# Kernel optimization log

Measured on AMD Instinct MI355X. Metric: run time of the kernel, lower is better.

Reference implementation:

```python
import jax, jax.numpy as jnp
import numpy as np

EPS = 1e-5


def setup_inputs() -> dict:
    key = jax.random.key(0)
    ks = jax.random.split(key, 7)
    N, M, D, H, DM = 8192, 128, 64, 8, 1024  # tokens, num_memories, d_memory, heads, d_model
    return {
        "query": jax.random.normal(ks[0], (N, DM), dtype=jnp.float32),
        "addresses": jax.random.normal(ks[1], (M, D), dtype=jnp.float32),
        "memories": jax.random.normal(ks[2], (N, M, D), dtype=jnp.float32),
        "Wq": jax.random.normal(ks[3], (DM, H * D), dtype=jnp.float32) / np.sqrt(DM),
        "bq": jax.random.normal(ks[4], (H * D,), dtype=jnp.float32) * 0.01,
        "Wo": jax.random.normal(ks[5], (H * D, DM), dtype=jnp.float32) / np.sqrt(H * D),
        "bo": jax.random.normal(ks[6], (DM,), dtype=jnp.float32) * 0.01,
    }


def reference(query, addresses, memories, Wq, bq, Wo, bo):
    N = query.shape[0]
    M, D = addresses.shape
    # Query projection -> heads: (N, H, D)
    q = (query @ Wq + bq).reshape(N, -1, D)
    q = jax.nn.relu(q)  # kernel feature map on query
    # Keys: memory content + learned addresses, kernel feature map
    k = jax.nn.relu(memories + addresses)  # (N, M, D)
    # make_kernel: contract over the num_memories dim
    matrix = jnp.einsum("nmd,nme->nde", k, memories)  # (N, D, D)
    normalizer = jnp.sum(k, axis=-2)  # (N, D)
    # read_from_kernel
    numerator = jnp.einsum("nhd,nde->nhe", q, matrix)  # (N, H, D)
    denominator = jnp.einsum("nhd,nd->nh", q, normalizer)[..., None] + EPS
    attn = numerator / denominator  # (N, H, D)
    # merge heads back to d_model
    return attn.reshape(N, -1) @ Wo + bo
```

## Files before the change

### kernel.cpp

```cpp
#include <hip/hip_runtime.h>

typedef __bf16 bf16x8 __attribute__((ext_vector_type(8)));
typedef __bf16 bf16x4 __attribute__((ext_vector_type(4)));
typedef __bf16 bf16x2 __attribute__((ext_vector_type(2)));
typedef float  f32x4  __attribute__((ext_vector_type(4)));

__device__ __forceinline__ void gload_lds16(const void* g, void* l) {
    auto gp = reinterpret_cast<const __attribute__((address_space(1))) unsigned int*>(
        reinterpret_cast<uintptr_t>(g));
    auto lp = reinterpret_cast<__attribute__((address_space(3))) unsigned int*>(
        reinterpret_cast<uintptr_t>(l));
    __builtin_amdgcn_global_load_lds(gp, lp, 16, 0, 0);
}

__device__ __forceinline__ void xcd_remap(int lin, int& bx, int& by) {
    const int wgid = (lin & 7) * 64 + (lin >> 3);
    bx = wgid & 7;
    by = wgid >> 3;
}

__global__ __launch_bounds__(256) void prep_all(
    const float* __restrict__ Wq, const float* __restrict__ Wo,
    const float* __restrict__ adr,
    __bf16* __restrict__ WqT, __bf16* __restrict__ WoT,
    __bf16* __restrict__ adrb)
{
    __shared__ float tile[32][33];
    const int bid = blockIdx.x, tid = threadIdx.x;

    if (bid < 1024) {
        const float* src; __bf16* dst; int R, C, r0, c0;
        if (bid < 512) {
            src = Wq; dst = WqT; R = 1024; C = 512;
            c0 = (bid & 15) * 32; r0 = (bid >> 4) * 32;
        } else {
            const int b = bid - 512;
            src = Wo; dst = WoT; R = 512; C = 1024;
            c0 = (b & 31) * 32; r0 = (b >> 5) * 32;
        }
        const int tx = tid & 31, ty = tid >> 5;
        #pragma unroll
        for (int i = ty; i < 32; i += 8)
            tile[i][tx] = src[(size_t)(r0 + i) * C + c0 + tx];
        __syncthreads();
        #pragma unroll
        for (int i = ty; i < 32; i += 8)
            dst[(size_t)(c0 + i) * R + r0 + tx] = (__bf16)tile[tx][i];
    } else {
        const int i = (bid - 1024) * 256 + tid;
        f32x4 a = ((const f32x4*)adr)[2 * i];
        f32x4 b = ((const f32x4*)adr)[2 * i + 1];
        bf16x8 o;
        #pragma unroll
        for (int j = 0; j < 4; ++j) { o[j] = (__bf16)a[j]; o[4 + j] = (__bf16)b[j]; }
        ((bf16x8*)adrb)[i] = o;
    }
}

__global__ __launch_bounds__(512) void gemm_qproj(
    const float* __restrict__ A, const __bf16* __restrict__ BT,
    const float* __restrict__ bias, __bf16* __restrict__ Out,
    int M, int N, int K)
{
    __shared__ __bf16 As[2][128][40];
    __shared__ __bf16 Bs[2][64][32];

    const int tid = threadIdx.x, lane = tid & 63, w = tid >> 6;
    const int wm = w >> 1, wn = w & 1;
    int bx, by;
    xcd_remap(blockIdx.x + 8 * blockIdx.y, bx, by);
    const int m0 = by * 128, n0 = bx * 64;
    const int r = lane & 15, g = lane >> 4;

    const int arow = tid >> 2, ac8 = (tid & 3) * 8;
    const float*  gA = A + (size_t)(m0 + arow) * K + ac8;
    const __bf16* gB = BT + (size_t)(n0 + 16 * w + (lane >> 2)) * K + (lane & 3) * 8;

    f32x4 acc[2][2];
    const f32x4 zero = {0.f, 0.f, 0.f, 0.f};
    #pragma unroll
    for (int mi = 0; mi < 2; ++mi)
        #pragma unroll
        for (int ni = 0; ni < 2; ++ni) acc[mi][ni] = zero;

    const int NT = K / 32;

    if (w < 4) gload_lds16(gB, &Bs[0][16 * w][0]);
    {
        const f32x4 la0 = *(const f32x4*)(gA);
        const f32x4 la1 = *(const f32x4*)(gA + 4);
        bf16x8 bl;
        #pragma unroll
        for (int j = 0; j < 4; ++j) { bl[j] = (__bf16)la0[j]; bl[4 + j] = (__bf16)la1[j]; }
        *(bf16x8*)&As[0][arow][ac8] = bl;
    }
    __syncthreads();

    int cur = 0;
    for (int t = 0; t < NT; ++t) {
        const int k0 = t * 32;
        f32x4 ln0, ln1;
        if (t + 1 < NT) {
            if (w < 4) gload_lds16(gB + k0 + 32, &Bs[cur ^ 1][16 * w][0]);
            ln0 = *(const f32x4*)(gA + k0 + 32);
            ln1 = *(const f32x4*)(gA + k0 + 36);
        }
        bf16x8 af[2], bfr[2];
        #pragma unroll
        for (int mi = 0; mi < 2; ++mi)
            af[mi] = *(const bf16x8*)&As[cur][wm * 32 + mi * 16 + r][g * 8];
        #pragma unroll
        for (int ni = 0; ni < 2; ++ni)
            bfr[ni] = *(const bf16x8*)&Bs[cur][wn * 32 + ni * 16 + r][g * 8];
        #pragma unroll
        for (int mi = 0; mi < 2; ++mi)
            #pragma unroll
            for (int ni = 0; ni < 2; ++ni)
                acc[mi][ni] = __builtin_amdgcn_mfma_f32_16x16x32_bf16(
                    af[mi], bfr[ni], acc[mi][ni], 0, 0, 0);
        if (t + 1 < NT) {
            bf16x8 bl;
            #pragma unroll
            for (int j = 0; j < 4; ++j) { bl[j] = (__bf16)ln0[j]; bl[4 + j] = (__bf16)ln1[j]; }
            *(bf16x8*)&As[cur ^ 1][arow][ac8] = bl;
        }
        __syncthreads();
        cur ^= 1;
    }

    const int orow = m0 + wm * 32 + g * 4;
    const int ocol = n0 + wn * 32 + r;
    #pragma unroll
    for (int ni = 0; ni < 2; ++ni) {
        const float bb = bias[ocol + ni * 16];
        #pragma unroll
        for (int mi = 0; mi < 2; ++mi) {
            #pragma unroll
            for (int q = 0; q < 4; ++q) {
                float v = fmaxf(acc[mi][ni][q] + bb, 0.f);
                Out[(size_t)(orow + mi * 16 + q) * N + ocol + ni * 16] = (__bf16)v;
            }
        }
    }
}

__global__ __launch_bounds__(512) void gemm_oproj(
    const __bf16* __restrict__ A, const __bf16* __restrict__ BT,
    const float* __restrict__ bias, float* __restrict__ Out,
    int M, int N, int K)
{
    __shared__ __bf16 As[2][128][32];
    __shared__ __bf16 Bs[2][128][32];

    const int tid = threadIdx.x, lane = tid & 63, w = tid >> 6;
    const int wm = w >> 1, wn = w & 1;
    int bx, by;
    xcd_remap(blockIdx.x + 8 * blockIdx.y, bx, by);
    const int m0 = by * 128, n0 = bx * 128;
    const int r = lane & 15, g = lane >> 4;

    const int srow = lane >> 2;
    const int scol = (lane & 3) * 8;
    const __bf16* gA = A  + (size_t)(m0 + 16 * w + srow) * K + scol;
    const __bf16* gB = BT + (size_t)(n0 + 16 * w + srow) * K + scol;

    f32x4 acc[2][4];
    const f32x4 zero = {0.f, 0.f, 0.f, 0.f};
    #pragma unroll
    for (int mi = 0; mi < 2; ++mi)
        #pragma unroll
        for (int ni = 0; ni < 4; ++ni) acc[mi][ni] = zero;

    const int NT = K / 32;

    gload_lds16(gA, &As[0][16 * w][0]);
    gload_lds16(gB, &Bs[0][16 * w][0]);
    __syncthreads();

    int cur = 0;
    for (int t = 0; t < NT; ++t) {
        const int k0 = t * 32;
        if (t + 1 < NT) {
            gload_lds16(gA + k0 + 32, &As[cur ^ 1][16 * w][0]);
            gload_lds16(gB + k0 + 32, &Bs[cur ^ 1][16 * w][0]);
        }
        bf16x8 af[2], bfr[4];
        #pragma unroll
        for (int mi = 0; mi < 2; ++mi)
            af[mi] = *(const bf16x8*)&As[cur][wm * 32 + mi * 16 + r][g * 8];
        #pragma unroll
        for (int ni = 0; ni < 4; ++ni)
            bfr[ni] = *(const bf16x8*)&Bs[cur][wn * 64 + ni * 16 + r][g * 8];
        #pragma unroll
        for (int mi = 0; mi < 2; ++mi)
            #pragma unroll
            for (int ni = 0; ni < 4; ++ni)
                acc[mi][ni] = __builtin_amdgcn_mfma_f32_16x16x32_bf16(
                    af[mi], bfr[ni], acc[mi][ni], 0, 0, 0);
        __syncthreads();
        cur ^= 1;
    }

    const int orow = m0 + wm * 32 + g * 4;
    const int ocol = n0 + wn * 64 + r;
    #pragma unroll
    for (int ni = 0; ni < 4; ++ni) {
        const float bb = bias[ocol + ni * 16];
        #pragma unroll
        for (int mi = 0; mi < 2; ++mi) {
            #pragma unroll
            for (int q = 0; q < 4; ++q) {
                Out[(size_t)(orow + mi * 16 + q) * N + ocol + ni * 16]
                    = acc[mi][ni][q] + bb;
            }
        }
    }
}

__device__ __forceinline__ int kbyte(int m, int e) {
    return m * 128 + ((((e >> 3) ^ (m & 7))) << 4) + (e & 7) * 2;
}

__global__ void memory_attn_mfma(
    const __bf16* __restrict__ Q,
    const float*  __restrict__ mem,
    const __bf16* __restrict__ adrb,
    __bf16* __restrict__ attn)
{
    __shared__ __align__(16) unsigned char kbuf[4][4096];
    __shared__ __align__(16) unsigned char tbuf[4][5120];
    __shared__ float denl[4][8];

    const int tid = threadIdx.x, lane = tid & 63, w = tid >> 6;
    const int n = blockIdx.x * 4 + w;
    const int v = lane & 15, g = lane >> 4;

    unsigned char* kb = kbuf[w];
    unsigned char* tb = tbuf[w];

    const __bf16* qp = Q + (size_t)n * 512 + v * 64 + 8 * g;
    const bf16x8 qf0 = *(const bf16x8*)(qp);
    const bf16x8 qf1 = *(const bf16x8*)(qp + 32);

    f32x4 acc[4];
    const f32x4 zero = {0.f, 0.f, 0.f, 0.f};
    #pragma unroll
    for (int nb = 0; nb < 4; ++nb) acc[nb] = zero;
    float psum = 0.f;

    for (int c = 0; c < 4; ++c) {
        const int mb = c * 32;
        #pragma unroll
        for (int i = 0; i < 4; ++i) {
            const int mo = 8 * i + 2 * g;
            const int e  = 4 * v;
            const float* pm = mem + (((size_t)n * 128 + mb + mo) * 64 + e);
            const f32x4 m0 = *(const f32x4*)pm;
            const f32x4 m1 = *(const f32x4*)(pm + 64);
            const bf16x4 a0 = *(const bf16x4*)(adrb + (size_t)(mb + mo) * 64 + e);
            const bf16x4 a1 = *(const bf16x4*)(adrb + (size_t)(mb + mo + 1) * 64 + e);
            bf16x4 k0, k1;
            #pragma unroll
            for (int j = 0; j < 4; ++j) {
                k0[j] = (__bf16)fmaxf(m0[j] + (float)a0[j], 0.f);
                k1[j] = (__bf16)fmaxf(m1[j] + (float)a1[j], 0.f);
            }
            *(bf16x4*)(kb + kbyte(mo,     e)) = k0;
            *(bf16x4*)(kb + kbyte(mo + 1, e)) = k1;
            const int kap = 8 * ((mo >> 2) & 3) + 4 * (mo >> 4) + (mo & 3);
            #pragma unroll
            for (int j2 = 0; j2 < 4; ++j2) {
                bf16x2 p = { (__bf16)m0[j2], (__bf16)m1[j2] };
                *(bf16x2*)(tb + (size_t)(e + j2) * 80 + kap * 2) = p;
            }
        }

        f32x4 sA0 = zero, sA1 = zero;
        {
            const bf16x8 a00 = *(const bf16x8*)(kb + kbyte(v,      8 * g));
            const bf16x8 a01 = *(const bf16x8*)(kb + kbyte(v,      32 + 8 * g));
            const bf16x8 a10 = *(const bf16x8*)(kb + kbyte(v + 16, 8 * g));
            const bf16x8 a11 = *(const bf16x8*)(kb + kbyte(v + 16, 32 + 8 * g));
            sA0 = __builtin_amdgcn_mfma_f32_16x16x32_bf16(a00, qf0, sA0, 0, 0, 0);
            sA0 = __builtin_amdgcn_mfma_f32_16x16x32_bf16(a01, qf1, sA0, 0, 0, 0);
            sA1 = __builtin_amdgcn_mfma_f32_16x16x32_bf16(a10, qf0, sA1, 0, 0, 0);
            sA1 = __builtin_amdgcn_mfma_f32_16x16x32_bf16(a11, qf1, sA1, 0, 0, 0);
        }
        psum += sA0[0] + sA0[1] + sA0[2] + sA0[3]
              + sA1[0] + sA1[1] + sA1[2] + sA1[3];

        bf16x8 pa;
        #pragma unroll
        for (int q = 0; q < 4; ++q) {
            pa[q]     = (__bf16)sA0[q];
            pa[4 + q] = (__bf16)sA1[q];
        }

        #pragma unroll
        for (int nb = 0; nb < 4; ++nb) {
            const bf16x8 bf = *(const bf16x8*)(tb + (size_t)(16 * nb + v) * 80 + 16 * g);
            acc[nb] = __builtin_amdgcn_mfma_f32_16x16x32_bf16(pa, bf, acc[nb], 0, 0, 0);
        }
    }

    psum += __shfl_xor(psum, 16);
    psum += __shfl_xor(psum, 32);
    if (lane < 8) denl[w][lane] = psum;

    if (g < 2) {
        const f32x4 d4 = *(const f32x4*)&denl[w][4 * g];
        float inv[4];
        #pragma unroll
        for (int q = 0; q < 4; ++q) inv[q] = 1.f / (d4[q] + 1e-5f);
        #pragma unroll
        for (int nb = 0; nb < 4; ++nb) {
            #pragma unroll
            for (int q = 0; q < 4; ++q) {
                attn[(size_t)n * 512 + (4 * g + q) * 64 + 16 * nb + v] =
                    (__bf16)(acc[nb][q] * inv[q]);
            }
        }
    }
}

extern "C" void kernel_launch(void* const* d_in, const int* in_sizes, int n_in,
                              void* d_out, int out_size, void* d_ws, size_t ws_size,
                              hipStream_t stream)
{
    const float* query     = (const float*)d_in[0];
    const float* addresses = (const float*)d_in[1];
    const float* memories  = (const float*)d_in[2];
    const float* Wq        = (const float*)d_in[3];
    const float* bq        = (const float*)d_in[4];
    const float* Wo        = (const float*)d_in[5];
    const float* bo        = (const float*)d_in[6];
    float* out = (float*)d_out;

    char* ws = (char*)d_ws;
    __bf16* WqT  = (__bf16*)(ws);
    __bf16* WoT  = (__bf16*)(ws + (1 << 20));
    __bf16* Qb   = (__bf16*)(ws + (2 << 20));
    __bf16* Ab   = (__bf16*)(ws + (10 << 20));
    __bf16* Adrb = (__bf16*)(ws + (18 << 20));

    prep_all<<<1028, 256, 0, stream>>>(Wq, Wo, addresses, WqT, WoT, Adrb);

    gemm_qproj<<<dim3(512 / 64, 8192 / 128), 512, 0, stream>>>(
        query, WqT, bq, Qb, 8192, 512, 1024);

    memory_attn_mfma<<<dim3(8192 / 4), 256, 0, stream>>>(Qb, memories, Adrb, Ab);

    gemm_oproj<<<dim3(1024 / 128, 8192 / 128), 512, 0, stream>>>(
        Ab, WoT, bo, out, 8192, 1024, 512);
}
```

Before: 113.8 us.

## Deepen prefetch pipelines in projection GEMMs with fine-grained waitcnt barriers

```diff
diff --git a/kernel.cpp b/kernel.cpp
--- a/kernel.cpp
+++ b/kernel.cpp
@@ -11,6 +11,25 @@
     auto lp = reinterpret_cast<__attribute__((address_space(3))) unsigned int*>(
         reinterpret_cast<uintptr_t>(l));
     __builtin_amdgcn_global_load_lds(gp, lp, 16, 0, 0);
+}
+
+__device__ __forceinline__ void barrier_lgkm() {
+    __builtin_amdgcn_sched_barrier(0);
+    asm volatile("s_waitcnt lgkmcnt(0)" ::: "memory");
+    __builtin_amdgcn_s_barrier();
+    __builtin_amdgcn_sched_barrier(0);
+}
+__device__ __forceinline__ void barrier_vm2_lgkm() {
+    __builtin_amdgcn_sched_barrier(0);
+    asm volatile("s_waitcnt vmcnt(2) lgkmcnt(0)" ::: "memory");
+    __builtin_amdgcn_s_barrier();
+    __builtin_amdgcn_sched_barrier(0);
+}
+__device__ __forceinline__ void barrier_vm0_lgkm() {
+    __builtin_amdgcn_sched_barrier(0);
+    asm volatile("s_waitcnt vmcnt(0) lgkmcnt(0)" ::: "memory");
+    __builtin_amdgcn_s_barrier();
+    __builtin_amdgcn_sched_barrier(0);
 }
 
 __device__ __forceinline__ void xcd_remap(int lin, int& bx, int& by) {
@@ -73,8 +92,10 @@
     const int r = lane & 15, g = lane >> 4;
 
     const int arow = tid >> 2, ac8 = (tid & 3) * 8;
-    const float*  gA = A + (size_t)(m0 + arow) * K + ac8;
-    const __bf16* gB = BT + (size_t)(n0 + 16 * w + (lane >> 2)) * K + (lane & 3) * 8;
+    const float* gA = A + (size_t)(m0 + arow) * K + ac8;
+    const bool bstage = (w < 4);
+    const int brow = 16 * (w & 3) + (lane >> 2), bc8 = (lane & 3) * 8;
+    const __bf16* gB = BT + (size_t)(n0 + brow) * K + bc8;
 
     f32x4 acc[2][2];
     const f32x4 zero = {0.f, 0.f, 0.f, 0.f};
@@ -85,33 +106,36 @@
 
     const int NT = K / 32;
 
-    if (w < 4) gload_lds16(gB, &Bs[0][16 * w][0]);
+    f32x4 pa0[2], pa1[2];
+    bf16x8 pb[2];
+
+    pa0[0] = *(const f32x4*)(gA);      pa1[0] = *(const f32x4*)(gA + 4);
+    pa0[1] = *(const f32x4*)(gA + 32); pa1[1] = *(const f32x4*)(gA + 36);
+    if (bstage) { pb[0] = *(const bf16x8*)(gB); pb[1] = *(const bf16x8*)(gB + 32); }
     {
-        const f32x4 la0 = *(const f32x4*)(gA);
-        const f32x4 la1 = *(const f32x4*)(gA + 4);
         bf16x8 bl;
         #pragma unroll
-        for (int j = 0; j < 4; ++j) { bl[j] = (__bf16)la0[j]; bl[4 + j] = (__bf16)la1[j]; }
+        for (int j = 0; j < 4; ++j) { bl[j] = (__bf16)pa0[0][j]; bl[4 + j] = (__bf16)pa1[0][j]; }
         *(bf16x8*)&As[0][arow][ac8] = bl;
-    }
-    __syncthreads();
-
-    int cur = 0;
+        if (bstage) *(bf16x8*)&Bs[0][brow][bc8] = pb[0];
+    }
+    barrier_lgkm();
+
+    #pragma unroll 2
     for (int t = 0; t < NT; ++t) {
-        const int k0 = t * 32;
-        f32x4 ln0, ln1;
-        if (t + 1 < NT) {
-            if (w < 4) gload_lds16(gB + k0 + 32, &Bs[cur ^ 1][16 * w][0]);
-            ln0 = *(const f32x4*)(gA + k0 + 32);
-            ln1 = *(const f32x4*)(gA + k0 + 36);
+        const int ph = t & 1;
+        if (t + 2 < NT) {
+            pa0[ph] = *(const f32x4*)(gA + (t + 2) * 32);
+            pa1[ph] = *(const f32x4*)(gA + (t + 2) * 32 + 4);
+            if (bstage) pb[ph] = *(const bf16x8*)(gB + (t + 2) * 32);
         }
         bf16x8 af[2], bfr[2];
         #pragma unroll
         for (int mi = 0; mi < 2; ++mi)
-            af[mi] = *(const bf16x8*)&As[cur][wm * 32 + mi * 16 + r][g * 8];
+            af[mi] = *(const bf16x8*)&As[ph][wm * 32 + mi * 16 + r][g * 8];
         #pragma unroll
         for (int ni = 0; ni < 2; ++ni)
-            bfr[ni] = *(const bf16x8*)&Bs[cur][wn * 32 + ni * 16 + r][g * 8];
+            bfr[ni] = *(const bf16x8*)&Bs[ph][wn * 32 + ni * 16 + r][g * 8];
         #pragma unroll
         for (int mi = 0; mi < 2; ++mi)
             #pragma unroll
@@ -121,11 +145,14 @@
         if (t + 1 < NT) {
             bf16x8 bl;
             #pragma unroll
-            for (int j = 0; j < 4; ++j) { bl[j] = (__bf16)ln0[j]; bl[4 + j] = (__bf16)ln1[j]; }
-            *(bf16x8*)&As[cur ^ 1][arow][ac8] = bl;
-        }
-        __syncthreads();
-        cur ^= 1;
+            for (int j = 0; j < 4; ++j) {
+                bl[j]     = (__bf16)pa0[ph ^ 1][j];
+                bl[4 + j] = (__bf16)pa1[ph ^ 1][j];
+            }
+            *(bf16x8*)&As[ph ^ 1][arow][ac8] = bl;
+            if (bstage) *(bf16x8*)&Bs[ph ^ 1][brow][bc8] = pb[ph ^ 1];
+        }
+        barrier_lgkm();
     }
 
     const int orow = m0 + wm * 32 + g * 4;
@@ -149,8 +176,8 @@
     const float* __restrict__ bias, float* __restrict__ Out,
     int M, int N, int K)
 {
-    __shared__ __bf16 As[2][128][32];
-    __shared__ __bf16 Bs[2][128][32];
+    __shared__ __bf16 As[3][128][32];
+    __shared__ __bf16 Bs[3][128][32];
 
     const int tid = threadIdx.x, lane = tid & 63, w = tid >> 6;
     const int wm = w >> 1, wn = w & 1;
@@ -173,32 +200,40 @@
 
     const int NT = K / 32;
 
-    gload_lds16(gA, &As[0][16 * w][0]);
-    gload_lds16(gB, &Bs[0][16 * w][0]);
-    __syncthreads();
-
-    int cur = 0;
+    gload_lds16(gA,      &As[0][16 * w][0]);
+    gload_lds16(gB,      &Bs[0][16 * w][0]);
+    gload_lds16(gA + 32, &As[1][16 * w][0]);
+    gload_lds16(gB + 32, &Bs[1][16 * w][0]);
+    __builtin_amdgcn_sched_barrier(0);
+    asm volatile("s_waitcnt vmcnt(2)" ::: "memory");
+    __builtin_amdgcn_s_barrier();
+    __builtin_amdgcn_sched_barrier(0);
+
+    int buf = 0;
     for (int t = 0; t < NT; ++t) {
-        const int k0 = t * 32;
-        if (t + 1 < NT) {
-            gload_lds16(gA + k0 + 32, &As[cur ^ 1][16 * w][0]);
-            gload_lds16(gB + k0 + 32, &Bs[cur ^ 1][16 * w][0]);
+        if (t + 2 < NT) {
+            const int nb = (buf + 2 >= 3) ? buf - 1 : buf + 2;
+            gload_lds16(gA + (t + 2) * 32, &As[nb][16 * w][0]);
+            gload_lds16(gB + (t + 2) * 32, &Bs[nb][16 * w][0]);
         }
         bf16x8 af[2], bfr[4];
         #pragma unroll
         for (int mi = 0; mi < 2; ++mi)
-            af[mi] = *(const bf16x8*)&As[cur][wm * 32 + mi * 16 + r][g * 8];
+            af[mi] = *(const bf16x8*)&As[buf][wm * 32 + mi * 16 + r][g * 8];
         #pragma unroll
         for (int ni = 0; ni < 4; ++ni)
-            bfr[ni] = *(const bf16x8*)&Bs[cur][wn * 64 + ni * 16 + r][g * 8];
+            bfr[ni] = *(const bf16x8*)&Bs[buf][wn * 64 + ni * 16 + r][g * 8];
         #pragma unroll
         for (int mi = 0; mi < 2; ++mi)
             #pragma unroll
             for (int ni = 0; ni < 4; ++ni)
                 acc[mi][ni] = __builtin_amdgcn_mfma_f32_16x16x32_bf16(
                     af[mi], bfr[ni], acc[mi][ni], 0, 0, 0);
-        __syncthreads();
-        cur ^= 1;
+        if (t + 1 < NT) {
+            if (t + 2 < NT) barrier_vm2_lgkm();
+            else            barrier_vm0_lgkm();
+        }
+        buf = (buf + 1 >= 3) ? 0 : buf + 1;
     }
 
     const int orow = m0 + wm * 32 + g * 4;
```

Measured after the change: 234.8 us. 106% more time.
